# Performance work log

Hardware: AMD Instinct MI355X
Metric: run time of the kernel (lower is better)

Reference implementation:

```python
import jax, jax.numpy as jnp
import numpy as np

BATCH = 8192
IN_DIM = 512
OUT_DIM = 512
GRID_SIZE = 5
SPLINE_ORDER = 3
# grid has 2*(G+K)+1 knots -> after K de Boor steps basis count = 2*G+K
N_BASES = 2 * GRID_SIZE + SPLINE_ORDER  # 13
CLAMP_EPS = 1e-4
DENOM_EPS = 1e-8


def _make_grid():
    step = 2.0 / GRID_SIZE
    g = jnp.arange(-GRID_SIZE - SPLINE_ORDER, GRID_SIZE + SPLINE_ORDER + 1, dtype=jnp.float32) * step
    return jnp.tile(g[None, :], (IN_DIM, 1))  # [in_dim, 2*(G+K)+1]


def _b_spline(x, grid):
    # x: [B, in], grid: [in, L] -> bases: [B, in, 2*G+K]
    xg = x[..., None]  # [B, in, 1]
    bases = ((xg >= grid[:, :-1]) & (xg < grid[:, 1:])).astype(x.dtype)
    for k in range(1, SPLINE_ORDER + 1):
        denom1 = grid[:, k:-1] - grid[:, :-(k + 1)] + DENOM_EPS
        left = (xg - grid[:, :-(k + 1)]) / denom1
        denom2 = grid[:, k + 1:] - grid[:, 1:-k] + DENOM_EPS
        right = (grid[:, k + 1:] - xg) / denom2
        bases = left * bases[..., :-1] + right * bases[..., 1:]
    return bases


def setup_inputs() -> dict:
    key = jax.random.key(0)
    k1, k2, k3 = jax.random.split(key, 3)
    x = jax.random.normal(k1, (BATCH, IN_DIM), dtype=jnp.float32)
    # kaiming_uniform(a=sqrt(5)) ~ U(-1/sqrt(fan_in), 1/sqrt(fan_in))
    b_c = 1.0 / np.sqrt(IN_DIM * N_BASES)
    coeffs = jax.random.uniform(k2, (OUT_DIM, IN_DIM, N_BASES), dtype=jnp.float32, minval=-b_c, maxval=b_c)
    b_w = 1.0 / np.sqrt(IN_DIM)
    base_weight = jax.random.uniform(k3, (OUT_DIM, IN_DIM), dtype=jnp.float32, minval=-b_w, maxval=b_w)
    return {"x": x, "coeffs": coeffs, "base_weight": base_weight}


def reference(x, coeffs, base_weight):
    grid = _make_grid()
    xc = jnp.clip(x, -1.0 + CLAMP_EPS, 1.0 - CLAMP_EPS)
    basis = _b_spline(xc, grid)                       # [B, in, nb]
    spline_out = jnp.einsum('oic,bic->bo', coeffs, basis)
    base_out = jax.nn.silu(x) @ base_weight.T         # F.linear(silu(x), W)
    y = spline_out + base_out + x                     # residual (in_dim == out_dim)
    return y
```

## Files before the change

### kernel.cpp

```cpp
#include <hip/hip_runtime.h>
#include <stdint.h>

typedef unsigned int u32;
typedef unsigned short u16;
typedef unsigned long long u64;
typedef __bf16 bf16x8 __attribute__((ext_vector_type(8)));
typedef float f32x4 __attribute__((ext_vector_type(4)));
typedef u32 u32x4 __attribute__((ext_vector_type(4)));

#define IN_DIM 512

__device__ __forceinline__ u16 bfr(float f) {
  __bf16 h = (__bf16)f;
  return __builtin_bit_cast(u16, h);
}
__device__ __forceinline__ u16 f2bf(float f) {
  u32 u = __builtin_bit_cast(u32, f);
  u += 0x7fffu + ((u >> 16) & 1u);
  return (u16)(u >> 16);
}
__device__ __forceinline__ u32 pk2(float a, float b) {
  return (u32)f2bf(a) | ((u32)f2bf(b) << 16);
}

__global__ void pack_b(const float* __restrict__ coeffs,
                       const float* __restrict__ bw,
                       char* __restrict__ Bp) {
  __shared__ float stage[64][56];
  const int tid = threadIdx.x;
  const int q = tid & 3, g = tid >> 2;
  const int id = blockIdx.x * 64 + g;
  const int col = id >> 7, s = id & 127;
  const float* cbase = coeffs + ((size_t)col * IN_DIM + s * 4) * 13;
#pragma unroll
  for (int j = 0; j < 3; ++j) {
    int ch = q + j * 4;
    float4 v = *(const float4*)(cbase + ch * 4);
    stage[g][ch * 4 + 0] = v.x; stage[g][ch * 4 + 1] = v.y;
    stage[g][ch * 4 + 2] = v.z; stage[g][ch * 4 + 3] = v.w;
  }
  if (q == 0) {
    float4 v = *(const float4*)(cbase + 48);
    stage[g][48] = v.x; stage[g][49] = v.y; stage[g][50] = v.z; stage[g][51] = v.w;
  }
  if (q == 1) {
    float4 v = *(const float4*)(bw + (size_t)col * IN_DIM + s * 4);
    stage[g][52] = v.x; stage[g][53] = v.y; stage[g][54] = v.z; stage[g][55] = v.w;
  }
  __syncthreads();
  const int nbp = col >> 7, cb = (col >> 4) & 7, cl = col & 15;
  char* base = Bp + (((size_t)(nbp * 128 + s) * 8 + cb) * 2) * 1024;
#pragma unroll
  for (int r = 0; r < 2; ++r) {
    int idx = q * 2 + r;
    int h = idx & 1;
    int dd = idx >> 1;
    int ks = dd >> 1;
    const float* sf = &stage[g][dd * 13];
    float w = stage[g][52 + dd];
    u16 hh[8];
#pragma unroll
    for (int c = 0; c < 8; ++c) {
      int slot = h * 8 + c;
      float v = slot < 13 ? sf[slot] : (slot < 15 ? w : 0.0f);
      hh[c] = bfr(v);
    }
    u32x4 o;
    o.x = (u32)hh[0] | ((u32)hh[1] << 16);
    o.y = (u32)hh[2] | ((u32)hh[3] << 16);
    o.z = (u32)hh[4] | ((u32)hh[5] << 16);
    o.w = (u32)hh[6] | ((u32)hh[7] << 16);
    int lanei = cl + 16 * (2 * (dd & 1) + h);
    *(u32x4*)(base + (size_t)ks * 1024 + lanei * 16) = o;
  }
}

__device__ __forceinline__ void expandA(float xv, char* rb, u32 swz, u32 k0) {
  float xc = fminf(fmaxf(xv, -0.9999f), 0.9999f);
  float tp = __fmaf_rn(xc, 2.5f, 3.0f);
  float fj = floorf(tp);
  int jl = (int)fj;
  float u = tp - fj;
  float u2 = u * u, u3 = u2 * u;
  float vv = 1.0f - u;
  float b0 = vv * vv * vv * (1.0f / 6.0f);
  float b3 = u3 * (1.0f / 6.0f);
  float b1 = __fmaf_rn(0.5f, u3, __fmaf_rn(u2, -1.0f, 2.0f / 3.0f));
  float b2 = 1.0f - b0 - b1 - b3;
  float e = __expf(-xv);
  float sg = __fdividef(xv, 1.0f + e);
  u16 sh = bfr(sg);
  float shf = __builtin_bit_cast(float, ((u32)sh) << 16);
  u16 sl = bfr(sg - shf);
  u32 pk01 = (u32)bfr(b0) | ((u32)bfr(b1) << 16);
  u32 pk23 = (u32)bfr(b2) | ((u32)bfr(b3) << 16);
  u64 v = (u64)pk01 | (((u64)pk23) << 32);
  int sstart = jl + 2;
  int qa = sstart >> 2;
  int shn = (sstart & 3) << 4;
  u64 lo = v << shn;
  u64 hi = shn ? (v >> (64 - shn)) : 0ull;
  u64 q0 = qa ? 0ull : lo;
  u64 q1 = qa ? lo : hi;
  u64 q2 = qa ? hi : 0ull;
  u64 q3 = (u64)(((u32)sh) << 16) | (((u64)(u32)sl) << 32);
  u32x4 c0, c1;
  c0.x = (u32)q0; c0.y = (u32)(q0 >> 32); c0.z = (u32)q1; c0.w = (u32)(q1 >> 32);
  c1.x = (u32)q2; c1.y = (u32)(q2 >> 32); c1.z = (u32)q3; c1.w = (u32)(q3 >> 32);
  *(u32x4*)(rb + ((k0 ^ swz) << 4)) = c0;
  *(u32x4*)(rb + (((k0 + 1u) ^ swz) << 4)) = c1;
}

#define MM(AF, BV)                                                             \
  {                                                                            \
    __builtin_amdgcn_s_setprio(1);                                             \
    _Pragma("unroll")                                                          \
    for (int fm = 0; fm < 4; ++fm)                                             \
      _Pragma("unroll")                                                        \
      for (int fn = 0; fn < 4; ++fn)                                           \
        acc[fm][fn] = __builtin_amdgcn_mfma_f32_16x16x32_bf16(                 \
            __builtin_bit_cast(bf16x8, AF[fm]),                                \
            __builtin_bit_cast(bf16x8, BV[fn]), acc[fm][fn], 0, 0, 0);         \
    __builtin_amdgcn_s_setprio(0);                                             \
  }

__launch_bounds__(768, 3)
__global__ void kan_gemm(const float* __restrict__ x,
                         const char* __restrict__ Bp,
                         float* __restrict__ out) {
  __shared__ __align__(16) char smem[131072];

  const int tid = threadIdx.x;
  const int lane = tid & 63;
  const int wid = tid >> 6;
  const bool isC = (wid < 8);

  const int kt = wid >> 2;
  const int wm = (wid >> 1) & 1, wn = wid & 1;
  const int lrow = lane & 15, lkg = lane >> 4;

  int s0 = blockIdx.x;
  int xcd = s0 & 7;
  int nb = xcd >> 1;
  int mb = ((s0 >> 3) << 1) | (xcd & 1);

  const int te = tid & 255;
  const int erow = te >> 2;
  const int ad = te & 3;
  const u32 aswz = (u32)(erow & 7);
  const u32 ak0 = (u32)(ad * 2);
  const float* xpa = x + (size_t)(mb * 128 + erow) * IN_DIM + ad;
  const float* xpb = xpa + (size_t)64 * IN_DIM;

  const char* bptr = Bp + (((size_t)(nb * 128) * 8 + wn * 4) * 2 + kt) * 1024 + (size_t)lane * 16;

  f32x4 acc[4][4];
#pragma unroll
  for (int i = 0; i < 4; ++i)
#pragma unroll
    for (int j = 0; j < 4; ++j) acc[i][j] = (f32x4){0.f, 0.f, 0.f, 0.f};

  u32x4 bA[4], bB[4];
  char* ab0 = smem;
  char* ab1 = smem + 65536;

  float xc[8];
#pragma unroll
  for (int j = 0; j < 8; ++j) xc[j] = 0.f;

  if (isC) {
#pragma unroll
    for (int fn = 0; fn < 4; ++fn)
      bA[fn] = *(const u32x4*)(bptr + fn * 2048);
  } else {
    float xi[8];
#pragma unroll
    for (int k = 0; k < 4; ++k) { xi[2 * k] = xpa[4 * k]; xi[2 * k + 1] = xpb[4 * k]; }
#pragma unroll
    for (int k = 0; k < 4; ++k) {
      expandA(xi[2 * k],     ab0 + k * 16384 + erow * 128, aswz, ak0);
      expandA(xi[2 * k + 1], ab0 + k * 16384 + (erow + 64) * 128, aswz, ak0);
    }
#pragma unroll
    for (int k = 0; k < 4; ++k) { xc[2 * k] = xpa[16 + 4 * k]; xc[2 * k + 1] = xpb[16 + 4 * k]; }
  }
  __syncthreads();

  const u32 asl = (((u32)(kt * 4) | (u32)lkg) ^ (u32)(lrow & 7)) << 4;

#pragma unroll 1
  for (int iv = 0; iv < 32; ++iv) {
    if (isC) {
      const char* rb = (iv & 1) ? ab1 : ab0;
      const char* arb = rb + (wm * 64 + lrow) * 128;
      const int S = iv * 4;
      u32x4 af0[4], af1[4];
#pragma unroll
      for (int fm = 0; fm < 4; ++fm)
        af0[fm] = *(const u32x4*)(arb + fm * 2048 + asl);
#pragma unroll
      for (int fm = 0; fm < 4; ++fm)
        af1[fm] = *(const u32x4*)(arb + 16384 + fm * 2048 + asl);
#pragma unroll
      for (int fn = 0; fn < 4; ++fn)
        bB[fn] = *(const u32x4*)(bptr + (size_t)(S + 1) * 16384 + fn * 2048);
      MM(af0, bA)
#pragma unroll
      for (int fm = 0; fm < 4; ++fm)
        af0[fm] = *(const u32x4*)(arb + 2 * 16384 + fm * 2048 + asl);
#pragma unroll
      for (int fn = 0; fn < 4; ++fn)
        bA[fn] = *(const u32x4*)(bptr + (size_t)(S + 2) * 16384 + fn * 2048);
      MM(af1, bB)
#pragma unroll
      for (int fm = 0; fm < 4; ++fm)
        af1[fm] = *(const u32x4*)(arb + 3 * 16384 + fm * 2048 + asl);
#pragma unroll
      for (int fn = 0; fn < 4; ++fn)
        bB[fn] = *(const u32x4*)(bptr + (size_t)(S + 3) * 16384 + fn * 2048);
      MM(af0, bA)
      {
        int sn = (S + 4 < 128) ? (S + 4) : 127;
#pragma unroll
        for (int fn = 0; fn < 4; ++fn)
          bA[fn] = *(const u32x4*)(bptr + (size_t)sn * 16384 + fn * 2048);
      }
      MM(af1, bB)
    } else {
      if (iv + 1 < 32) {
        char* wb = (iv & 1) ? ab0 : ab1;
#pragma unroll
        for (int k = 0; k < 4; ++k) {
          expandA(xc[2 * k],     wb + k * 16384 + erow * 128, aswz, ak0);
          expandA(xc[2 * k + 1], wb + k * 16384 + (erow + 64) * 128, aswz, ak0);
        }
      }
      {
        int v2 = (iv + 2 < 32) ? (iv + 2) : 31;
        float xn[8];
#pragma unroll
        for (int k = 0; k < 4; ++k) {
          xn[2 * k]     = xpa[v2 * 16 + 4 * k];
          xn[2 * k + 1] = xpb[v2 * 16 + 4 * k];
        }
#pragma unroll
        for (int j = 0; j < 8; ++j) xc[j] = xn[j];
      }
      asm volatile("s_waitcnt lgkmcnt(0)" ::: "memory");
    }
    __builtin_amdgcn_s_barrier();
  }

  __syncthreads();

  float* red = (float*)smem;
  if (isC && kt == 1) {
#pragma unroll
    for (int fm = 0; fm < 4; ++fm)
#pragma unroll
      for (int fn = 0; fn < 4; ++fn) {
        int rr = wm * 64 + fm * 16 + lkg * 4;
        int cc = wn * 64 + fn * 16 + lrow;
#pragma unroll
        for (int r = 0; r < 4; ++r)
          red[(size_t)(rr + r) * 132 + cc] = acc[fm][fn][r];
      }
  }
  __syncthreads();
  if (isC && kt == 0) {
#pragma unroll
    for (int fm = 0; fm < 4; ++fm)
#pragma unroll
      for (int fn = 0; fn < 4; ++fn) {
        int rr = wm * 64 + fm * 16 + lkg * 4;
        int cc = wn * 64 + fn * 16 + lrow;
        size_t gb = (size_t)(mb * 128 + rr) * IN_DIM + nb * 128 + cc;
#pragma unroll
        for (int r = 0; r < 4; ++r) {
          size_t off = gb + (size_t)r * IN_DIM;
          out[off] = acc[fm][fn][r] + red[(size_t)(rr + r) * 132 + cc] + x[off];
        }
      }
  }
}

__device__ __forceinline__ void st_b16(char* rb, u32 swz, u32 k0, int c, u16 v) {
  u32 uc = (u32)c;
  u32 byte = (((k0 + (uc >> 3)) ^ swz) << 4) | ((uc & 7u) << 1);
  *(u16*)(rb + byte) = v;
}

__device__ __forceinline__ void stage_a_fb(char* aT, int row, int d, float xv) {
  char* rb = aT + row * 128;
  u32 swz = (u32)(row & 7);
  float xc = fminf(fmaxf(xv, -0.9999f), 0.9999f);
  float tp = __fmaf_rn(xc, 2.5f, 3.0f);
  float fj = floorf(tp);
  int jl = (int)fj;
  float u = tp - fj;
  float u2 = u * u, u3 = u2 * u;
  float vv = 1.0f - u;
  float b0 = vv * vv * vv * (1.0f / 6.0f);
  float b3 = u3 * (1.0f / 6.0f);
  float b1 = __fmaf_rn(0.5f, u3, __fmaf_rn(u2, -1.0f, 2.0f / 3.0f));
  float b2 = 1.0f - b0 - b1 - b3;
  float e = __expf(-xv);
  float sg = __fdividef(xv, 1.0f + e);
  u16 sh = f2bf(sg);
  float shf = __builtin_bit_cast(float, ((u32)sh) << 16);
  u16 slo = f2bf(sg - shf);
  u32 k0 = (u32)d * 2u;
  u32x4 z = {0u, 0u, 0u, 0u};
  *(u32x4*)(rb + ((k0 ^ swz) << 4)) = z;
  u32x4 z2 = {0u, 0u, ((u32)sh) << 16, (u32)slo};
  *(u32x4*)(rb + (((k0 + 1u) ^ swz) << 4)) = z2;
  st_b16(rb, swz, k0, jl + 2, f2bf(b0));
  st_b16(rb, swz, k0, jl + 3, f2bf(b1));
  st_b16(rb, swz, k0, jl + 4, f2bf(b2));
  st_b16(rb, swz, k0, jl + 5, f2bf(b3));
}

__launch_bounds__(512, 2)
__global__ void kan_fused(const float* __restrict__ x,
                          const float* __restrict__ coeffs,
                          const float* __restrict__ bw,
                          float* __restrict__ out) {
  __shared__ __align__(16) char smem[65536];
  const int tid = threadIdx.x;
  const int lane = tid & 63;
  const int wid = tid >> 6;
  const int team = wid >> 2;
  const int wm = (wid >> 1) & 1;
  const int wn = wid & 1;
  const int m0 = wm * 64, n0 = wn * 64;
  const int lrow = lane & 15;
  const int lkg = lane >> 4;
  int s = blockIdx.x;
  int xcd = s & 7;
  int nb = xcd >> 1;
  int mb = (s >> 3) | ((xcd & 1) << 5);
  const int t = tid & 255;
  const int arow = t >> 1;
  const int h = t & 1;
  char* aT = smem + team * 16384;
  char* bT = smem + 32768 + team * 16384;
  const int dim0 = team * 256;
  const float* xptr = x + (size_t)(mb * 128 + arow) * IN_DIM + dim0 + 2 * h;
  const float* cptr = coeffs + ((size_t)((nb * 128 + arow) * IN_DIM) + dim0) * 13 + 26 * h;
  const float* wptr = bw + (size_t)(nb * 128 + arow) * IN_DIM + dim0 + 2 * h;
  f32x4 acc[4][4];
#pragma unroll
  for (int i = 0; i < 4; ++i)
#pragma unroll
    for (int j = 0; j < 4; ++j) acc[i][j] = (f32x4){0.f, 0.f, 0.f, 0.f};
  float2 xv, wv;
  float2 cv0, cv1, cv2, cv3, cv4, cv5, cv6, cv7, cv8, cv9, cv10, cv11, cv12;
#define PREFETCH(STP)                                                     \
  {                                                                       \
    const float* cp_ = cptr + (STP) * 52;                                 \
    xv = *(const float2*)(xptr + (STP) * 4);                              \
    wv = *(const float2*)(wptr + (STP) * 4);                              \
    cv0 = *(const float2*)(cp_ + 0);   cv1 = *(const float2*)(cp_ + 2);   \
    cv2 = *(const float2*)(cp_ + 4);   cv3 = *(const float2*)(cp_ + 6);   \
    cv4 = *(const float2*)(cp_ + 8);   cv5 = *(const float2*)(cp_ + 10);  \
    cv6 = *(const float2*)(cp_ + 12);  cv7 = *(const float2*)(cp_ + 14);  \
    cv8 = *(const float2*)(cp_ + 16);  cv9 = *(const float2*)(cp_ + 18);  \
    cv10 = *(const float2*)(cp_ + 20); cv11 = *(const float2*)(cp_ + 22); \
    cv12 = *(const float2*)(cp_ + 24);                                    \
  }
  PREFETCH(0)
  for (int st = 0; st < 64; ++st) {
    stage_a_fb(aT, arow, 2 * h + 0, xv.x);
    stage_a_fb(aT, arow, 2 * h + 1, xv.y);
    {
      char* rb = bT + arow * 128;
      u32 swz = (u32)(arow & 7);
      u32 k0 = (u32)(2 * h) * 2u;
      u32x4 lo, hi;
      lo.x = pk2(cv0.x, cv0.y); lo.y = pk2(cv1.x, cv1.y);
      lo.z = pk2(cv2.x, cv2.y); lo.w = pk2(cv3.x, cv3.y);
      hi.x = pk2(cv4.x, cv4.y); hi.y = pk2(cv5.x, cv5.y);
      {
        u16 wb = f2bf(wv.x);
        hi.z = (u32)f2bf(cv6.x) | ((u32)wb << 16);
        hi.w = (u32)wb;
      }
      *(u32x4*)(rb + ((k0 ^ swz) << 4)) = lo;
      *(u32x4*)(rb + (((k0 + 1u) ^ swz) << 4)) = hi;
      lo.x = pk2(cv6.y, cv7.x);  lo.y = pk2(cv7.y, cv8.x);
      lo.z = pk2(cv8.y, cv9.x);  lo.w = pk2(cv9.y, cv10.x);
      hi.x = pk2(cv10.y, cv11.x); hi.y = pk2(cv11.y, cv12.x);
      {
        u16 wb = f2bf(wv.y);
        hi.z = (u32)f2bf(cv12.y) | ((u32)wb << 16);
        hi.w = (u32)wb;
      }
      *(u32x4*)(rb + (((k0 + 2u) ^ swz) << 4)) = lo;
      *(u32x4*)(rb + (((k0 + 3u) ^ swz) << 4)) = hi;
    }
    __syncthreads();
    if (st != 63) { PREFETCH(st + 1) }
    {
      const char* arb = aT + (m0 + lrow) * 128;
      const char* brb = bT + (n0 + lrow) * 128;
      u32 rsw = (u32)(lrow & 7);
#pragma unroll
      for (int ks = 0; ks < 2; ++ks) {
        u32 sl2 = (((u32)(ks * 4) | (u32)lkg) ^ rsw) << 4;
        bf16x8 af[4], bfr2[4];
#pragma unroll
        for (int fm = 0; fm < 4; ++fm)
          af[fm] = __builtin_bit_cast(bf16x8, *(const u32x4*)(arb + fm * 2048 + sl2));
#pragma unroll
        for (int fn = 0; fn < 4; ++fn)
          bfr2[fn] = __builtin_bit_cast(bf16x8, *(const u32x4*)(brb + fn * 2048 + sl2));
#pragma unroll
        for (int fm = 0; fm < 4; ++fm)
#pragma unroll
          for (int fn = 0; fn < 4; ++fn)
            acc[fm][fn] = __builtin_amdgcn_mfma_f32_16x16x32_bf16(
                af[fm], bfr2[fn], acc[fm][fn], 0, 0, 0);
      }
    }
    __syncthreads();
  }
  float* red = (float*)smem;
  if (team == 1) {
#pragma unroll
    for (int fm = 0; fm < 4; ++fm)
#pragma unroll
      for (int fn = 0; fn < 4; ++fn) {
        int rr = m0 + fm * 16 + lkg * 4;
        int cc = n0 + fn * 16 + lrow;
#pragma unroll
        for (int r = 0; r < 4; ++r) red[(rr + r) * 128 + cc] = acc[fm][fn][r];
      }
  }
  __syncthreads();
  if (team == 0) {
#pragma unroll
    for (int fm = 0; fm < 4; ++fm)
#pragma unroll
      for (int fn = 0; fn < 4; ++fn) {
        int rr = m0 + fm * 16 + lkg * 4;
        int ccol = n0 + fn * 16 + lrow;
        int grow = mb * 128 + rr;
        int gcol = nb * 128 + ccol;
#pragma unroll
        for (int r = 0; r < 4; ++r) {
          float v = acc[fm][fn][r] + red[(rr + r) * 128 + ccol] +
                    x[(size_t)(grow + r) * IN_DIM + gcol];
          out[(size_t)(grow + r) * IN_DIM + gcol] = v;
        }
      }
  }
}

extern "C" void kernel_launch(void* const* d_in, const int* in_sizes, int n_in,
                              void* d_out, int out_size, void* d_ws, size_t ws_size,
                              hipStream_t stream) {
  const float* x = (const float*)d_in[0];
  const float* coeffs = (const float*)d_in[1];
  const float* bw = (const float*)d_in[2];
  float* out = (float*)d_out;
  if (ws_size >= (size_t)512 * 16384) {
    char* Bp = (char*)d_ws;
    hipLaunchKernelGGL(pack_b, dim3(1024), dim3(256), 0, stream, coeffs, bw, Bp);
    hipLaunchKernelGGL(kan_gemm, dim3(256), dim3(768), 0, stream, x, Bp, out);
  } else {
    hipLaunchKernelGGL(kan_fused, dim3(256), dim3(512), 0, stream, x, coeffs, bw, out);
  }
}
```

Baseline: 89.21 us.

## Precompute expanded A operand in workspace and stream it from global in GEMM

Adds an expand_a kernel that writes the bf16 B-spline and SiLU expansion of x into a 128 MB workspace in MFMA fragment layout. A new kan_gemm2 then loads both A and B fragments straight from global memory into registers, removing the in-kernel expansion producer warps and the LDS staging. This path runs only when the workspace is large enough. The trade is a large extra write and read of A through HBM in place of on-the-fly ALU work that overlapped the GEMM.

New measurement: 126.7 us. 42.0% more time.

```diff
diff --git a/kernel.cpp b/kernel.cpp
--- a/kernel.cpp
+++ b/kernel.cpp
@@ -72,6 +72,164 @@
     o.w = (u32)hh[6] | ((u32)hh[7] << 16);
     int lanei = cl + 16 * (2 * (dd & 1) + h);
     *(u32x4*)(base + (size_t)ks * 1024 + lanei * 16) = o;
+  }
+}
+
+__device__ __forceinline__ u32x4 expandHalf(float xv, int h) {
+  float xc = fminf(fmaxf(xv, -0.9999f), 0.9999f);
+  float tp = __fmaf_rn(xc, 2.5f, 3.0f);
+  float fj = floorf(tp);
+  int jl = (int)fj;
+  float u = tp - fj;
+  float u2 = u * u, u3 = u2 * u;
+  float vv = 1.0f - u;
+  float b0 = vv * vv * vv * (1.0f / 6.0f);
+  float b3 = u3 * (1.0f / 6.0f);
+  float b1 = __fmaf_rn(0.5f, u3, __fmaf_rn(u2, -1.0f, 2.0f / 3.0f));
+  float b2 = 1.0f - b0 - b1 - b3;
+  float e = __expf(-xv);
+  float sg = __fdividef(xv, 1.0f + e);
+  u16 sh = bfr(sg);
+  float shf = __builtin_bit_cast(float, ((u32)sh) << 16);
+  u16 sl = bfr(sg - shf);
+  u32 pk01 = (u32)bfr(b0) | ((u32)bfr(b1) << 16);
+  u32 pk23 = (u32)bfr(b2) | ((u32)bfr(b3) << 16);
+  u64 v = (u64)pk01 | (((u64)pk23) << 32);
+  int sstart = jl + 2;
+  int qa = sstart >> 2;
+  int shn = (sstart & 3) << 4;
+  u64 lo = v << shn;
+  u64 hi = shn ? (v >> (64 - shn)) : 0ull;
+  u64 q0 = qa ? 0ull : lo;
+  u64 q1 = qa ? lo : hi;
+  u64 q2 = qa ? hi : 0ull;
+  u64 q3 = (u64)(((u32)sh) << 16) | (((u64)(u32)sl) << 32);
+  u64 ra = h ? q2 : q0;
+  u64 rb = h ? q3 : q1;
+  u32x4 r;
+  r.x = (u32)ra; r.y = (u32)(ra >> 32);
+  r.z = (u32)rb; r.w = (u32)(rb >> 32);
+  return r;
+}
+
+__global__ void expand_a(const float* __restrict__ x, char* __restrict__ Ap) {
+  const int tid = threadIdx.x;
+  const int lane = tid & 63;
+  const int wid = tid >> 6;
+  const int c = blockIdx.x * 4 + wid;
+  const int rbk = c & 511;
+  const int sk = c >> 9;
+  const int row = rbk * 16 + (lane & 15);
+  const int lkg = lane >> 4;
+  const int dim = 2 * sk + (lkg >> 1);
+  const int h = lkg & 1;
+  float xv = x[(size_t)row * IN_DIM + dim];
+  u32x4 r = expandHalf(xv, h);
+  *(u32x4*)(Ap + (size_t)c * 1024 + lane * 16) = r;
+}
+
+#define MM(AF, BV)                                                             \
+  {                                                                            \
+    __builtin_amdgcn_s_setprio(1);                                             \
+    _Pragma("unroll")                                                          \
+    for (int fm = 0; fm < 4; ++fm)                                             \
+      _Pragma("unroll")                                                        \
+      for (int fn = 0; fn < 4; ++fn)                                           \
+        acc[fm][fn] = __builtin_amdgcn_mfma_f32_16x16x32_bf16(                 \
+            __builtin_bit_cast(bf16x8, AF[fm]),                                \
+            __builtin_bit_cast(bf16x8, BV[fn]), acc[fm][fn], 0, 0, 0);         \
+    __builtin_amdgcn_s_setprio(0);                                             \
+  }
+
+__launch_bounds__(512, 2)
+__global__ void kan_gemm2(const float* __restrict__ x,
+                          const char* __restrict__ Ap,
+                          const char* __restrict__ Bp,
+                          float* __restrict__ out) {
+  __shared__ __align__(16) char smem[67584];
+
+  const int tid = threadIdx.x;
+  const int lane = tid & 63;
+  const int wid = tid >> 6;
+  const int kt = wid >> 2;
+  const int wm = (wid >> 1) & 1, wn = wid & 1;
+  const int lrow = lane & 15, lkg = lane >> 4;
+
+  int s0 = blockIdx.x;
+  int xcd = s0 & 7;
+  int nb = xcd >> 1;
+  int mb = ((s0 >> 3) << 1) | (xcd & 1);
+
+  const int rb = mb * 8 + wm * 4;
+
+  const char* abase = Ap + (((size_t)kt * 512 + rb) * 1024) + (size_t)lane * 16;
+  const char* bptr = Bp + (((size_t)(nb * 128) * 8 + wn * 4) * 2 + kt) * 1024 + (size_t)lane * 16;
+
+  f32x4 acc[4][4];
+#pragma unroll
+  for (int i = 0; i < 4; ++i)
+#pragma unroll
+    for (int j = 0; j < 4; ++j) acc[i][j] = (f32x4){0.f, 0.f, 0.f, 0.f};
+
+  u32x4 bA[4], bB[4], afA[4], afB[4];
+
+#pragma unroll
+  for (int fm = 0; fm < 4; ++fm)
+    afA[fm] = *(const u32x4*)(abase + fm * 1024);
+#pragma unroll
+  for (int fn = 0; fn < 4; ++fn)
+    bA[fn] = *(const u32x4*)(bptr + fn * 2048);
+
+#define STEP2(S, AFC, AFN, BCUR, BNXT)                                         \
+  {                                                                            \
+    int sl_ = (S) + 1 < 128 ? (S) + 1 : 127;                                   \
+    const char* ap_ = abase + (size_t)sl_ * 1048576;                           \
+    const char* bp_ = bptr + (size_t)sl_ * 16384;                              \
+    _Pragma("unroll")                                                          \
+    for (int fn = 0; fn < 4; ++fn)                                             \
+      BNXT[fn] = *(const u32x4*)(bp_ + fn * 2048);                             \
+    _Pragma("unroll")                                                          \
+    for (int fm = 0; fm < 4; ++fm)                                             \
+      AFN[fm] = *(const u32x4*)(ap_ + fm * 1024);                              \
+    MM(AFC, BCUR)                                                              \
+  }
+
+#pragma unroll 1
+  for (int s = 0; s < 128; s += 2) {
+    STEP2(s, afA, afB, bA, bB)
+    STEP2(s + 1, afB, afA, bB, bA)
+  }
+
+  __syncthreads();
+
+  float* red = (float*)smem;
+  if (kt == 1) {
+#pragma unroll
+    for (int fm = 0; fm < 4; ++fm)
+#pragma unroll
+      for (int fn = 0; fn < 4; ++fn) {
+        int rr = wm * 64 + fm * 16 + lkg * 4;
+        int cc = wn * 64 + fn * 16 + lrow;
+#pragma unroll
+        for (int r = 0; r < 4; ++r)
+          red[(size_t)(rr + r) * 132 + cc] = acc[fm][fn][r];
+      }
+  }
+  __syncthreads();
+  if (kt == 0) {
+#pragma unroll
+    for (int fm = 0; fm < 4; ++fm)
+#pragma unroll
+      for (int fn = 0; fn < 4; ++fn) {
+        int rr = wm * 64 + fm * 16 + lkg * 4;
+        int cc = wn * 64 + fn * 16 + lrow;
+        size_t gb = (size_t)(mb * 128 + rr) * IN_DIM + nb * 128 + cc;
+#pragma unroll
+        for (int r = 0; r < 4; ++r) {
+          size_t off = gb + (size_t)r * IN_DIM;
+          out[off] = acc[fm][fn][r] + red[(size_t)(rr + r) * 132 + cc] + x[off];
+        }
+      }
   }
 }
 
@@ -111,19 +269,6 @@
   *(u32x4*)(rb + (((k0 + 1u) ^ swz) << 4)) = c1;
 }
 
-#define MM(AF, BV)                                                             \
-  {                                                                            \
-    __builtin_amdgcn_s_setprio(1);                                             \
-    _Pragma("unroll")                                                          \
-    for (int fm = 0; fm < 4; ++fm)                                             \
-      _Pragma("unroll")                                                        \
-      for (int fn = 0; fn < 4; ++fn)                                           \
-        acc[fm][fn] = __builtin_amdgcn_mfma_f32_16x16x32_bf16(                 \
-            __builtin_bit_cast(bf16x8, AF[fm]),                                \
-            __builtin_bit_cast(bf16x8, BV[fn]), acc[fm][fn], 0, 0, 0);         \
-    __builtin_amdgcn_s_setprio(0);                                             \
-  }
-
 __launch_bounds__(768, 3)
 __global__ void kan_gemm(const float* __restrict__ x,
                          const char* __restrict__ Bp,
@@ -191,8 +336,8 @@
 #pragma unroll 1
   for (int iv = 0; iv < 32; ++iv) {
     if (isC) {
-      const char* rb = (iv & 1) ? ab1 : ab0;
-      const char* arb = rb + (wm * 64 + lrow) * 128;
+      const char* rbuf = (iv & 1) ? ab1 : ab0;
+      const char* arb = rbuf + (wm * 64 + lrow) * 128;
       const int S = iv * 4;
       u32x4 af0[4], af1[4];
 #pragma unroll
@@ -463,7 +608,15 @@
   const float* coeffs = (const float*)d_in[1];
   const float* bw = (const float*)d_in[2];
   float* out = (float*)d_out;
-  if (ws_size >= (size_t)512 * 16384) {
+  const size_t B_BYTES = (size_t)8 << 20;
+  const size_t A_BYTES = (size_t)128 << 20;
+  if (ws_size >= B_BYTES + A_BYTES) {
+    char* Bp = (char*)d_ws;
+    char* Ap = (char*)d_ws + B_BYTES;
+    hipLaunchKernelGGL(pack_b, dim3(1024), dim3(256), 0, stream, coeffs, bw, Bp);
+    hipLaunchKernelGGL(expand_a, dim3(32768), dim3(256), 0, stream, x, Ap);
+    hipLaunchKernelGGL(kan_gemm2, dim3(256), dim3(512), 0, stream, x, Ap, Bp, out);
+  } else if (ws_size >= B_BYTES) {
     char* Bp = (char*)d_ws;
     hipLaunchKernelGGL(pack_b, dim3(1024), dim3(256), 0, stream, coeffs, bw, Bp);
     hipLaunchKernelGGL(kan_gemm, dim3(256), dim3(768), 0, stream, x, Bp, out);
```
